# Kernel tuning notes

Measured on AMD Instinct MI355X. Metric: run time of the kernel, lower is better.

## Reference

```python
import jax, jax.numpy as jnp
import numpy as np

B, SQ, SK, D, H, F = 8, 512, 1024, 1024, 16, 4096
DK = D // H
NEG_INF = -jnp.inf


def _linear(x, w, b):
    return x @ w + b


def _mha(q, k, v, wq, bq, wk, bk, wv, bv, wo, bo, causal, kv_mask):
    # q: [B,Sq,D], k/v: [B,Sk,D]
    b, sq, d = q.shape
    sk = k.shape[1]
    Q = _linear(q, wq, bq).reshape(b, sq, H, DK).transpose(0, 2, 1, 3)  # [B,H,Sq,dk]
    K = _linear(k, wk, bk).reshape(b, sk, H, DK).transpose(0, 2, 1, 3)
    V = _linear(v, wv, bv).reshape(b, sk, H, DK).transpose(0, 2, 1, 3)
    S = jnp.einsum('bhqd,bhkd->bhqk', Q, K) / jnp.sqrt(jnp.asarray(DK, Q.dtype))
    if kv_mask is not None:
        S = jnp.where(kv_mask[:, None, None, :] == 0, NEG_INF, S)
    if causal:
        tri = jnp.tril(jnp.ones((sq, sk), dtype=bool))
        S = jnp.where(tri, S, NEG_INF)
    A = jax.nn.softmax(S, axis=-1)  # dropout p=0 -> identity
    x = jnp.einsum('bhqk,bhkd->bhqd', A, V).transpose(0, 2, 1, 3).reshape(b, sq, d)
    return _linear(x, wo, bo), A


def _ln(x, g, beta, eps=1e-5):
    mu = jnp.mean(x, axis=-1, keepdims=True)
    var = jnp.mean(jnp.square(x - mu), axis=-1, keepdims=True)
    return (x - mu) * jax.lax.rsqrt(var + eps) * g + beta


def setup_inputs() -> dict:
    key = jax.random.key(0)
    ks = jax.random.split(key, 32)
    s = 0.02
    inp = {
        'x': jax.random.normal(ks[0], (B, SQ, D), jnp.float32),
        'enc_o': jax.random.normal(ks[1], (B, SK, D), jnp.float32),
        'enc_mask': jax.random.randint(ks[2], (B, SK), 0, 2, jnp.int32),
    }
    i = 3
    for pfx in ('a1', 'a2'):
        for nm in ('wq', 'wk', 'wv', 'wo'):
            inp[f'{pfx}_{nm}'] = jax.random.normal(ks[i], (D, D), jnp.float32) * s; i += 1
            inp[f'{pfx}_{nm[1:] and "b" + nm[1:]}'] = jnp.zeros((D,), jnp.float32)
    inp['ff_w1'] = jax.random.normal(ks[i], (D, F), jnp.float32) * s; i += 1
    inp['ff_b1'] = jnp.zeros((F,), jnp.float32)
    inp['ff_w2'] = jax.random.normal(ks[i], (F, D), jnp.float32) * s; i += 1
    inp['ff_b2'] = jnp.zeros((D,), jnp.float32)
    for n in ('ln1', 'ln2', 'ln3'):
        inp[f'{n}_g'] = jnp.ones((D,), jnp.float32)
        inp[f'{n}_b'] = jnp.zeros((D,), jnp.float32)
    return inp


def reference(x, enc_o, enc_mask,
              a1_wq, a1_bq, a1_wk, a1_bk, a1_wv, a1_bv, a1_wo, a1_bo,
              a2_wq, a2_bq, a2_wk, a2_bk, a2_wv, a2_bv, a2_wo, a2_bo,
              ff_w1, ff_b1, ff_w2, ff_b2,
              ln1_g, ln1_b, ln2_g, ln2_b, ln3_g, ln3_b):
    res, _ = _mha(x, x, x, a1_wq, a1_bq, a1_wk, a1_bk, a1_wv, a1_bv, a1_wo, a1_bo,
                  causal=True, kv_mask=None)
    x = _ln(x + res, ln1_g, ln1_b)
    res, attn = _mha(x, enc_o, enc_o, a2_wq, a2_bq, a2_wk, a2_bk, a2_wv, a2_bv, a2_wo, a2_bo,
                     causal=False, kv_mask=enc_mask)
    x = _ln(x + res, ln2_g, ln2_b)
    res = _linear(jax.nn.relu(_linear(x, ff_w1, ff_b1)), ff_w2, ff_b2)
    x = _ln(x + res, ln3_g, ln3_b)
    return (x, attn)
```

## Files before the change

### kernel.cpp

```cpp
#include <hip/hip_runtime.h>
#include <hip/hip_bf16.h>


using bf16 = __hip_bfloat16;
typedef __attribute__((ext_vector_type(8))) short short8;
typedef __attribute__((ext_vector_type(4))) float f32x4;

#define DEVINL __device__ __forceinline__

DEVINL unsigned short bf16bits(float f) {
  __hip_bfloat16 h = __float2bfloat16(f);
  return *reinterpret_cast<unsigned short*>(&h);
}
DEVINL float bits2f(unsigned short u) {
  return __uint_as_float(((unsigned int)u) << 16);
}
DEVINL float tofloat(float f) { return f; }
DEVINL float tofloat(bf16 h) { return __bfloat162float(h); }

#define GLD16(gp, lp) __builtin_amdgcn_global_load_lds( \
    (__attribute__((address_space(1))) const void*)(gp), \
    (__attribute__((address_space(3))) void*)(lp), 16, 0, 0)

struct GemmP {
  const bf16* A; const bf16* Bt; void* C;
  const float* bias; const int* kmask;
  float scale;
  int M, N, K, lda, ldb, ldc;
  long sAb, sAh, sBb, sBh, sCb, sCh;
};

enum { EPI_BIAS_BF16 = 0, EPI_CAUSAL_BF16, EPI_KMASK_F32, EPI_NONE_BF16,
       EPI_BIAS_F32, EPI_BIAS_RELU_BF16, EPI_PART_F32 };

template<int EPI>
DEVINL void gemm_body(const GemmP& p, int bx, int by, int bz) {
  __shared__ bf16 As[128 * 32];
  __shared__ bf16 Bs[128 * 32];
  const int t = threadIdx.x;
  const int lane = t & 63;
  const int w = t >> 6;
  const int zb = bz >> 4, zh = bz & 15;
  const int m0 = by * 128, n0 = bx * 128;

  const bf16* Ab = p.A + (long)zb * p.sAb + (long)zh * p.sAh;
  const bf16* Bb = p.Bt + (long)zb * p.sBb + (long)zh * p.sBh;
  const int fl = lane & 15, fq = lane >> 4;
  const int wm = (w >> 1) * 64, wn = (w & 1) * 64;

  f32x4 acc[4][4];
#pragma unroll
  for (int i = 0; i < 4; ++i)
#pragma unroll
    for (int j = 0; j < 4; ++j) acc[i][j] = (f32x4){0.f, 0.f, 0.f, 0.f};

  const int sr = t >> 2;
  const int sc = (t & 3) * 8;
  char* ldsA = (char*)As + w * 1024;
  char* ldsB = (char*)Bs + w * 1024;

  int brow0 = n0 + sr;      if (brow0 > p.N - 1) brow0 = p.N - 1;
  int brow1 = n0 + sr + 64; if (brow1 > p.N - 1) brow1 = p.N - 1;

  for (int k0 = 0; k0 < p.K; k0 += 32) {
    GLD16(Ab + (long)(m0 + sr) * p.lda + k0 + sc, ldsA);
    GLD16(Ab + (long)(m0 + sr + 64) * p.lda + k0 + sc, ldsA + 4096);
    GLD16(Bb + (long)brow0 * p.ldb + k0 + sc, ldsB);
    GLD16(Bb + (long)brow1 * p.ldb + k0 + sc, ldsB + 4096);
    __syncthreads();

    short8 af[4], bfv[4];
#pragma unroll
    for (int i = 0; i < 4; ++i)
      af[i] = *(const short8*)(As + (wm + i * 16 + fl) * 32 + fq * 8);
#pragma unroll
    for (int j = 0; j < 4; ++j)
      bfv[j] = *(const short8*)(Bs + (wn + j * 16 + fl) * 32 + fq * 8);
#pragma unroll
    for (int i = 0; i < 4; ++i)
#pragma unroll
      for (int j = 0; j < 4; ++j)
        acc[i][j] = __builtin_amdgcn_mfma_f32_16x16x32_bf16(af[i], bfv[j], acc[i][j], 0, 0, 0);
    __syncthreads();
  }

  const float NEGINF = -__builtin_inff();
  const long cbase = (long)zb * p.sCb + (long)zh * p.sCh;
#pragma unroll
  for (int i = 0; i < 4; ++i) {
#pragma unroll
    for (int j = 0; j < 4; ++j) {
#pragma unroll
      for (int r = 0; r < 4; ++r) {
        int row = m0 + wm + i * 16 + fq * 4 + r;
        int col = n0 + wn + j * 16 + fl;
        if (col < p.N) {
          float v = acc[i][j][r];
          if (EPI == EPI_BIAS_BF16 || EPI == EPI_BIAS_F32 || EPI == EPI_BIAS_RELU_BF16)
            v += p.bias[col];
          if (EPI == EPI_BIAS_RELU_BF16) v = v > 0.f ? v : 0.f;
          if (EPI == EPI_CAUSAL_BF16) { v *= p.scale; if (col > row) v = NEGINF; }
          if (EPI == EPI_KMASK_F32)   { v *= p.scale; if (p.kmask[zb * 1024 + col] == 0) v = NEGINF; }
          long off = cbase + (long)row * p.ldc + col;
          if (EPI == EPI_KMASK_F32 || EPI == EPI_BIAS_F32 || EPI == EPI_PART_F32)
            ((float*)p.C)[off] = v;
          else ((bf16*)p.C)[off] = __float2bfloat16(v);
        }
      }
    }
  }
}

template<int EPI>
__global__ __launch_bounds__(256)
void gemm_k(GemmP p) {
  gemm_body<EPI>(p, blockIdx.x, blockIdx.y, blockIdx.z);
}

struct Gemm2P { GemmP a, b; int nA, axw, bxw; };
__global__ __launch_bounds__(256)
void gemm2_k(Gemm2P q) {
  const int b = blockIdx.x;
  if (b < q.nA) gemm_body<EPI_BIAS_BF16>(q.a, b % q.axw, b / q.axw, 0);
  else { const int c = b - q.nA; gemm_body<EPI_BIAS_BF16>(q.b, c % q.bxw, c / q.bxw, 0); }
}

struct AttnP {
  const bf16 *Q, *K, *Vt;
  float* Pout; bf16* O;
  const int* kmask;
  int ldq, ldk, ldv;
  long sQb, sQh, sKb, sKh, sVb, sVh, sPb, sPh, sOb, sOh;
};

template<int SK, bool CAUSAL, bool WRITE_P>
__global__ __launch_bounds__(512)
void attn_fused_k(AttnP p) {
  constexpr int TKMAX = SK / 64;
  __shared__ bf16 S[64 * SK];
  __shared__ bf16 ring[3 * 4096];
  const int t = threadIdx.x;
  const int lane = t & 63;
  const int w = t >> 6;
  const int fl = lane & 15, fq = lane >> 4;
  const int qh = w >> 2;
  const int wc = w & 3;
  const int zb = blockIdx.z >> 4, zh = blockIdx.z & 15;
  const int q0 = blockIdx.y * 64;
  const float NEGINF = -__builtin_inff();

  const bf16* Qb = p.Q + (long)zb * p.sQb + (long)zh * p.sQh;
  const bf16* Kb = p.K + (long)zb * p.sKb + (long)zh * p.sKh;
  const bf16* Vb = p.Vt + (long)zb * p.sVb + (long)zh * p.sVh;

  const int Tk = CAUSAL ? (q0 >> 6) + 1 : TKMAX;

  short8 af[2][2];
#pragma unroll
  for (int i = 0; i < 2; ++i)
#pragma unroll
    for (int kk = 0; kk < 2; ++kk)
      af[i][kk] = *(const short8*)(Qb + (long)(q0 + qh * 32 + i * 16 + fl) * p.ldq + kk * 32 + fq * 8);

  int kmv[CAUSAL ? 1 : TKMAX];
  if (!CAUSAL) {
#pragma unroll
    for (int kt = 0; kt < TKMAX; ++kt)
      kmv[kt] = p.kmask[zb * 1024 + kt * 64 + wc * 16 + fl];
  }

  const int so = t * 16;
  const int srow = so >> 7;
  const int scb = (so & 127) ^ ((srow & 7) << 4);
  auto stage = [&](const bf16* mb, int ld, int roff, int coff, int buf) {
    GLD16(mb + (long)(roff + srow) * ld + coff + (scb >> 1),
          (char*)ring + buf * 8192 + so);
  };

  stage(Kb, p.ldk, 0, 0, 0);
  if (Tk > 1) stage(Kb, p.ldk, 64, 0, 1);
  for (int kt = 0; kt < Tk; ++kt) {
    if (kt + 1 < Tk) asm volatile("s_waitcnt vmcnt(1)" ::: "memory");
    else             asm volatile("s_waitcnt vmcnt(0)" ::: "memory");
    __builtin_amdgcn_s_barrier();
    if (kt + 2 < Tk) stage(Kb, p.ldk, (kt + 2) * 64, 0, (kt + 2) % 3);

    const char* kb = (const char*)ring + (kt % 3) * 8192;
    const int krow = wc * 16 + fl;
    short8 bfv[2];
#pragma unroll
    for (int kk = 0; kk < 2; ++kk)
      bfv[kk] = *(const short8*)(kb + ((krow * 128 + kk * 64 + fq * 16) ^ ((krow & 7) << 4)));
    f32x4 acc[2] = {(f32x4){0.f,0.f,0.f,0.f}, (f32x4){0.f,0.f,0.f,0.f}};
#pragma unroll
    for (int kk = 0; kk < 2; ++kk) {
      acc[0] = __builtin_amdgcn_mfma_f32_16x16x32_bf16(af[0][kk], bfv[kk], acc[0], 0, 0, 0);
      acc[1] = __builtin_amdgcn_mfma_f32_16x16x32_bf16(af[1][kk], bfv[kk], acc[1], 0, 0, 0);
    }
    const int col = kt * 64 + wc * 16 + fl;
    const bool mok = CAUSAL || (kmv[CAUSAL ? 0 : kt] != 0);
#pragma unroll
    for (int i = 0; i < 2; ++i) {
#pragma unroll
      for (int r = 0; r < 4; ++r) {
        int row = qh * 32 + i * 16 + fq * 4 + r;
        float v = acc[i][r] * 0.125f;
        if (CAUSAL) { if (col > q0 + row) v = NEGINF; }
        else if (!mok) v = NEGINF;
        int b = ((row * SK + col) * 2) ^ ((row & 7) << 4);
        *(bf16*)((char*)S + b) = __float2bfloat16(v);
      }
    }
  }
  asm volatile("s_waitcnt lgkmcnt(0)" ::: "memory");
  __builtin_amdgcn_s_barrier();

  const int Tv = Tk;
  stage(Vb, p.ldv, 0, 0, 0);
  if (Tv > 1) stage(Vb, p.ldv, 0, 64, 1);

  float* Pf = WRITE_P ? (p.Pout + (long)zb * p.sPb + (long)zh * p.sPh) : nullptr;
  constexpr int NC = SK / 512;
  const int lim = Tk * 64;
  for (int rr = 0; rr < 8; ++rr) {
    const int row = w * 8 + rr;
    const int swz = (row & 7) << 4;
    float fv[NC][8];
#pragma unroll
    for (int c = 0; c < NC; ++c) {
      const int col = c * 512 + lane * 8;
      if (!CAUSAL || col < lim) {
        short8 sv = *(const short8*)((char*)S + (((row * SK + col) * 2) ^ swz));
#pragma unroll
        for (int j = 0; j < 8; ++j) fv[c][j] = bits2f((unsigned short)sv[j]);
      } else {
#pragma unroll
        for (int j = 0; j < 8; ++j) fv[c][j] = NEGINF;
      }
    }
    float mx = fv[0][0];
#pragma unroll
    for (int c = 0; c < NC; ++c)
#pragma unroll
      for (int j = 0; j < 8; ++j) mx = fmaxf(mx, fv[c][j]);
    for (int off = 32; off; off >>= 1) mx = fmaxf(mx, __shfl_xor(mx, off, 64));
    float s = 0.f;
#pragma unroll
    for (int c = 0; c < NC; ++c)
#pragma unroll
      for (int j = 0; j < 8; ++j) { fv[c][j] = expf(fv[c][j] - mx); s += fv[c][j]; }
    for (int off = 32; off; off >>= 1) s += __shfl_xor(s, off, 64);
    const float inv = 1.f / s;
#pragma unroll
    for (int c = 0; c < NC; ++c) {
      const int col = c * 512 + lane * 8;
      if (!CAUSAL || col < lim) {
        short8 o;
#pragma unroll
        for (int j = 0; j < 8; ++j) o[j] = (short)bf16bits(fv[c][j] * inv);
        *(short8*)((char*)S + (((row * SK + col) * 2) ^ swz)) = o;
        if (WRITE_P) {
          float* pp = Pf + (long)(q0 + row) * SK + col;
          f32x4 o0, o1;
#pragma unroll
          for (int j = 0; j < 4; ++j) { o0[j] = fv[c][j] * inv; o1[j] = fv[c][4 + j] * inv; }
          *(f32x4*)pp = o0;
          *(f32x4*)(pp + 4) = o1;
        }
      }
    }
  }
  asm volatile("s_waitcnt lgkmcnt(0)" ::: "memory");
  __builtin_amdgcn_s_barrier();

  f32x4 ao[2] = {(f32x4){0.f,0.f,0.f,0.f}, (f32x4){0.f,0.f,0.f,0.f}};
  for (int vt = 0; vt < Tv; ++vt) {
    if (vt + 1 < Tv) asm volatile("s_waitcnt vmcnt(1)" ::: "memory");
    else             asm volatile("s_waitcnt vmcnt(0)" ::: "memory");
    __builtin_amdgcn_s_barrier();
    if (vt + 2 < Tv) stage(Vb, p.ldv, 0, (vt + 2) * 64, (vt + 2) % 3);

    const char* vbuf = (const char*)ring + (vt % 3) * 8192;
    const int vrow = wc * 16 + fl;
    short8 bv[2];
#pragma unroll
    for (int kk = 0; kk < 2; ++kk)
      bv[kk] = *(const short8*)(vbuf + ((vrow * 128 + kk * 64 + fq * 16) ^ ((vrow & 7) << 4)));
#pragma unroll
    for (int i = 0; i < 2; ++i) {
      const int row = qh * 32 + i * 16 + fl;
#pragma unroll
      for (int kk = 0; kk < 2; ++kk) {
        const int col = vt * 64 + kk * 32 + fq * 8;
        short8 pa = *(const short8*)((char*)S + (((row * SK + col) * 2) ^ ((row & 7) << 4)));
        ao[i] = __builtin_amdgcn_mfma_f32_16x16x32_bf16(pa, bv[kk], ao[i], 0, 0, 0);
      }
    }
  }

  bf16* Ob_ = p.O + (long)zb * p.sOb + (long)zh * p.sOh;
#pragma unroll
  for (int i = 0; i < 2; ++i)
#pragma unroll
    for (int r = 0; r < 4; ++r) {
      int row = q0 + qh * 32 + i * 16 + fq * 4 + r;
      Ob_[(long)row * 1024 + wc * 16 + fl] = __float2bfloat16(ao[i][r]);
    }
}

template<int NP>
__global__ __launch_bounds__(256)
void ln_fuse_k(const float* __restrict__ x, const float* __restrict__ part, long pstride,
               const float* __restrict__ pb,
               const float* __restrict__ g, const float* __restrict__ bt,
               float* __restrict__ outf, bf16* __restrict__ outb) {
  const int lane = threadIdx.x & 63;
  const long row = (long)blockIdx.x * 4 + (threadIdx.x >> 6);
  const float* px = x + row * 1024;
  float4 v[4];
  float s = 0.f;
#pragma unroll
  for (int c = 0; c < 4; ++c) {
    const int col = c * 256 + lane * 4;
    float4 a = *(const float4*)(px + col);
    float4 bb = *(const float4*)(pb + col);
    v[c].x = a.x + bb.x; v[c].y = a.y + bb.y; v[c].z = a.z + bb.z; v[c].w = a.w + bb.w;
#pragma unroll
    for (int sl = 0; sl < NP; ++sl) {
      float4 pp = *(const float4*)(part + sl * pstride + row * 1024 + col);
      v[c].x += pp.x; v[c].y += pp.y; v[c].z += pp.z; v[c].w += pp.w;
    }
    s += v[c].x + v[c].y + v[c].z + v[c].w;
  }
  for (int off = 32; off; off >>= 1) s += __shfl_xor(s, off, 64);
  float mu = s * (1.f / 1024.f);
  float q = 0.f;
#pragma unroll
  for (int c = 0; c < 4; ++c) {
    float dx = v[c].x - mu, dy = v[c].y - mu, dz = v[c].z - mu, dw = v[c].w - mu;
    q += dx * dx + dy * dy + dz * dz + dw * dw;
  }
  for (int off = 32; off; off >>= 1) q += __shfl_xor(q, off, 64);
  float rs = rsqrtf(q * (1.f / 1024.f) + 1e-5f);
#pragma unroll
  for (int c = 0; c < 4; ++c) {
    int col = c * 256 + lane * 4;
    float4 gg = *(const float4*)(g + col);
    float4 bb = *(const float4*)(bt + col);
    float4 o;
    o.x = (v[c].x - mu) * rs * gg.x + bb.x;
    o.y = (v[c].y - mu) * rs * gg.y + bb.y;
    o.z = (v[c].z - mu) * rs * gg.z + bb.z;
    o.w = (v[c].w - mu) * rs * gg.w + bb.w;
    *(float4*)(outf + row * 1024 + col) = o;
    if (outb) {
      uint2 pk;
      pk.x = bf16bits(o.x) | ((unsigned)bf16bits(o.y) << 16);
      pk.y = bf16bits(o.z) | ((unsigned)bf16bits(o.w) << 16);
      *(uint2*)(outb + row * 1024 + col) = pk;
    }
  }
}

template<typename TI>
DEVINL void tr_body(const TI* __restrict__ pin, bf16* __restrict__ pout,
                    int ldi, int ldo, int c0, int r0, int t, float tile[32][33]) {
  const int tx = t & 31, ty = t >> 5;
#pragma unroll
  for (int i = 0; i < 32; i += 8)
    tile[ty + i][tx] = tofloat(pin[(long)(r0 + ty + i) * ldi + c0 + tx]);
  __syncthreads();
#pragma unroll
  for (int i = 0; i < 32; i += 8)
    pout[(long)(c0 + ty + i) * ldo + r0 + tx] = __float2bfloat16(tile[tx][ty + i]);
}

struct PrepP {
  const float *x, *enc;
  const float* wsrc[10];
  const float *b0, *b1, *b2, *b4, *b5;
  bf16 *xb, *encb, *wT;
  float *bqkv, *bkv;
};
__global__ __launch_bounds__(256)
void prep_k(PrepP p) {
  __shared__ float tile[32][33];
  const int b = blockIdx.x, t = threadIdx.x;
  if (b < 12288) {
    const float* src = (b < 4096) ? p.x : p.enc;
    bf16* dst = (b < 4096) ? p.xb : p.encb;
    long i = (long)(b < 4096 ? b : b - 4096) * 256 + t;
    float4 v = *(const float4*)(src + i * 4);
    uint2 pk;
    pk.x = bf16bits(v.x) | ((unsigned)bf16bits(v.y) << 16);
    pk.y = bf16bits(v.z) | ((unsigned)bf16bits(v.w) << 16);
    *(uint2*)(dst + i * 4) = pk;
  } else if (b < 20480) {
    int l = b - 12288; int wdx = l >> 10; l &= 1023;
    tr_body<float>(p.wsrc[wdx], p.wT + (long)wdx * 1048576, 1024, 1024,
                   (l & 31) * 32, (l >> 5) * 32, t, tile);
  } else if (b < 24576) {
    int l = b - 20480;
    tr_body<float>(p.wsrc[8], p.wT + 8l * 1048576, 4096, 1024,
                   (l & 127) * 32, (l >> 7) * 32, t, tile);
  } else if (b < 28672) {
    int l = b - 24576;
    tr_body<float>(p.wsrc[9], p.wT + 12l * 1048576, 1024, 4096,
                   (l % 32) * 32, (l / 32) * 32, t, tile);
  } else if (b < 28684) {
    int i = (b - 28672) * 256 + t;
    p.bqkv[i] = (i < 1024) ? p.b0[i] : (i < 2048 ? p.b1[i - 1024] : p.b2[i - 2048]);
  } else {
    int i = (b - 28684) * 256 + t;
    p.bkv[i] = (i < 1024) ? p.b4[i] : p.b5[i - 1024];
  }
}

struct Vt2P { const bf16 *vs, *vc; bf16 *vts, *vtc; };
__global__ __launch_bounds__(256)
void vt2_k(Vt2P p) {
  __shared__ float tile[32][33];
  const int b = blockIdx.x, t = threadIdx.x;
  if (b < 4096) {
    int z = b >> 5, l = b & 31;
    int zb = z >> 4, zh = z & 15;
    tr_body<bf16>(p.vs + (long)zb * 1572864 + zh * 64,
                  p.vts + (long)zb * 524288 + zh * 32768,
                  3072, 512, (l & 1) * 32, (l >> 1) * 32, t, tile);
  } else {
    int c = b - 4096;
    int z = c >> 6, l = c & 63;
    int zb = z >> 4, zh = z & 15;
    tr_body<bf16>(p.vc + (long)zb * 2097152 + zh * 64,
                  p.vtc + (long)zb * 1048576 + zh * 65536,
                  2048, 1024, (l & 1) * 32, (l >> 1) * 32, t, tile);
  }
}

static inline GemmP mkp(const void* A, const bf16* Bt, void* C,
                        const float* bias, const int* km, float sc,
                        int M, int N, int K, int lda, int ldb, int ldc,
                        long sAb, long sAh, long sBb, long sBh, long sCb, long sCh) {
  GemmP p;
  p.A = (const bf16*)A; p.Bt = Bt; p.C = C; p.bias = bias; p.kmask = km; p.scale = sc;
  p.M = M; p.N = N; p.K = K; p.lda = lda; p.ldb = ldb; p.ldc = ldc;
  p.sAb = sAb; p.sAh = sAh; p.sBb = sBb; p.sBh = sBh; p.sCb = sCb; p.sCh = sCh;
  return p;
}

extern "C" void kernel_launch(void* const* d_in, const int* in_sizes, int n_in,
                              void* d_out, int out_size, void* d_ws, size_t ws_size,
                              hipStream_t stream) {
  const float* x        = (const float*)d_in[0];
  const float* enc_o    = (const float*)d_in[1];
  const int*   enc_mask = (const int*)d_in[2];
  const float* a1_wq = (const float*)d_in[3];  const float* a1_bq = (const float*)d_in[4];
  const float* a1_wk = (const float*)d_in[5];  const float* a1_bk = (const float*)d_in[6];
  const float* a1_wv = (const float*)d_in[7];  const float* a1_bv = (const float*)d_in[8];
  const float* a1_wo = (const float*)d_in[9];  const float* a1_bo = (const float*)d_in[10];
  const float* a2_wq = (const float*)d_in[11]; const float* a2_bq = (const float*)d_in[12];
  const float* a2_wk = (const float*)d_in[13]; const float* a2_bk = (const float*)d_in[14];
  const float* a2_wv = (const float*)d_in[15]; const float* a2_bv = (const float*)d_in[16];
  const float* a2_wo = (const float*)d_in[17]; const float* a2_bo = (const float*)d_in[18];
  const float* ff_w1 = (const float*)d_in[19]; const float* ff_b1 = (const float*)d_in[20];
  const float* ff_w2 = (const float*)d_in[21]; const float* ff_b2 = (const float*)d_in[22];
  const float* ln1_g = (const float*)d_in[23]; const float* ln1_b = (const float*)d_in[24];
  const float* ln2_g = (const float*)d_in[25]; const float* ln2_b = (const float*)d_in[26];
  const float* ln3_g = (const float*)d_in[27]; const float* ln3_b = (const float*)d_in[28];

  const size_t MB = 1u << 20;
  const long M1 = 1048576;
  char* w = (char*)d_ws;
  bf16*  xb   = (bf16*)(w + 0);
  bf16*  encb = (bf16*)(w + 8 * MB);
  float* x1f  = (float*)(w + 24 * MB);
  float* x2f  = (float*)(w + 40 * MB);
  bf16*  xcb  = (bf16*)(w + 56 * MB);
  bf16*  wT   = (bf16*)(w + 64 * MB);
  float* bqkv = (float*)(w + 96 * MB);
  float* bkv  = (float*)(w + 96 * MB + 16384);
  bf16*  QKV  = (bf16*)(w + 104 * MB);
  bf16*  KVc  = (bf16*)(w + 128 * MB);
  bf16*  VtS  = (bf16*)(w + 160 * MB);
  bf16*  Ob   = (bf16*)(w + 176 * MB);
  float* part = (float*)(w + 200 * MB);
  bf16*  Asf  = (bf16*)(w + 264 * MB);
  bf16*  VtC  = (bf16*)(w + 332 * MB);

  float* out_x = (float*)d_out;
  float* attn  = (float*)d_out + 4194304;

  const dim3 blk(256);
  const dim3 blk5(512);

  {
    PrepP pp;
    pp.x = x; pp.enc = enc_o;
    pp.wsrc[0] = a1_wq; pp.wsrc[1] = a1_wk; pp.wsrc[2] = a1_wv; pp.wsrc[3] = a1_wo;
    pp.wsrc[4] = a2_wq; pp.wsrc[5] = a2_wk; pp.wsrc[6] = a2_wv; pp.wsrc[7] = a2_wo;
    pp.wsrc[8] = ff_w1; pp.wsrc[9] = ff_w2;
    pp.b0 = a1_bq; pp.b1 = a1_bk; pp.b2 = a1_bv; pp.b4 = a2_bk; pp.b5 = a2_bv;
    pp.xb = xb; pp.encb = encb; pp.wT = wT; pp.bqkv = bqkv; pp.bkv = bkv;
    prep_k<<<28692, blk, 0, stream>>>(pp);
  }

  {
    Gemm2P q;
    q.a = mkp(xb, wT, QKV, bqkv, nullptr, 0.f, 4096, 3072, 1024, 1024, 1024, 3072, 0,0,0,0,0,0);
    q.b = mkp(encb, wT + 5 * M1, KVc, bkv, nullptr, 0.f, 8192, 2048, 1024, 1024, 1024, 2048, 0,0,0,0,0,0);
    q.nA = 768; q.axw = 24; q.bxw = 16;
    gemm2_k<<<1792, blk, 0, stream>>>(q);
  }
  bf16* Qs = QKV;
  bf16* Ks = QKV + 1024;
  bf16* Vs = QKV + 2048;
  bf16* Kc = KVc;
  bf16* Vc = KVc + 1024;

  {
    Vt2P vp; vp.vs = Vs; vp.vc = Vc; vp.vts = VtS; vp.vtc = VtC;
    vt2_k<<<12288, blk, 0, stream>>>(vp);
  }

  {
    AttnP ap;
    ap.Q = Qs; ap.K = Ks; ap.Vt = VtS; ap.Pout = nullptr; ap.O = Ob; ap.kmask = nullptr;
    ap.ldq = 3072; ap.ldk = 3072; ap.ldv = 512;
    ap.sQb = 1572864; ap.sQh = 64; ap.sKb = 1572864; ap.sKh = 64;
    ap.sVb = 524288;  ap.sVh = 32768; ap.sPb = 0; ap.sPh = 0;
    ap.sOb = 524288;  ap.sOh = 64;
    attn_fused_k<512, true, false><<<dim3(1, 8, 128), blk5, 0, stream>>>(ap);
  }

  gemm_k<EPI_PART_F32><<<dim3(8, 32, 2), blk, 0, stream>>>(
      mkp(Ob, wT + 3 * M1, part, nullptr, nullptr, 0.f, 4096, 1024, 512, 1024, 1024, 1024,
          0, 512, 0, 512, 0, 4194304));

  ln_fuse_k<2><<<1024, blk, 0, stream>>>(x, part, 4194304, a1_bo, ln1_g, ln1_b, x1f, xcb);

  gemm_k<EPI_BIAS_BF16><<<dim3(8, 32, 1), blk, 0, stream>>>(
      mkp(xcb, wT + 4 * M1, QKV, a2_bq, nullptr, 0.f, 4096, 1024, 1024, 1024, 1024, 1024, 0,0,0,0,0,0));
  bf16* Qc = QKV;

  {
    AttnP ap;
    ap.Q = Qc; ap.K = Kc; ap.Vt = VtC; ap.Pout = attn; ap.O = Ob; ap.kmask = enc_mask;
    ap.ldq = 1024; ap.ldk = 2048; ap.ldv = 1024;
    ap.sQb = 524288;  ap.sQh = 64; ap.sKb = 2097152; ap.sKh = 64;
    ap.sVb = 1048576; ap.sVh = 65536; ap.sPb = 8388608; ap.sPh = 524288;
    ap.sOb = 524288;  ap.sOh = 64;
    attn_fused_k<1024, false, true><<<dim3(1, 8, 128), blk5, 0, stream>>>(ap);
  }

  gemm_k<EPI_PART_F32><<<dim3(8, 32, 2), blk, 0, stream>>>(
      mkp(Ob, wT + 7 * M1, part, nullptr, nullptr, 0.f, 4096, 1024, 512, 1024, 1024, 1024,
          0, 512, 0, 512, 0, 4194304));

  ln_fuse_k<2><<<1024, blk, 0, stream>>>(x1f, part, 4194304, a2_bo, ln2_g, ln2_b, x2f, xcb);

  gemm_k<EPI_BIAS_RELU_BF16><<<dim3(32, 32, 1), blk, 0, stream>>>(
      mkp(xcb, wT + 8 * M1, Asf, ff_b1, nullptr, 0.f, 4096, 4096, 1024, 1024, 1024, 4096, 0,0,0,0,0,0));

  gemm_k<EPI_PART_F32><<<dim3(8, 32, 4), blk, 0, stream>>>(
      mkp(Asf, wT + 12 * M1, part, nullptr, nullptr, 0.f, 4096, 1024, 1024, 4096, 4096, 1024,
          0, 1024, 0, 1024, 0, 4194304));

  ln_fuse_k<4><<<1024, blk, 0, stream>>>(x2f, part, 4194304, ff_b2, ln3_g, ln3_b, out_x, nullptr);
}
```

Baseline: 988.8 us.

## Halve attention query tile, remap grid across XCDs, use nontemporal stores for P

Each attention block now handles 32 query rows instead of 64. This halves the shared score buffer and cuts the K/V ring from triple to double buffering, so more blocks can be resident per CU. The launch becomes a 1D grid of 2048 blocks, remapped so that neighbouring heads and tiles are spread across XCDs. The fp32 attention-probability output now uses nontemporal stores. The cost is that each K/V tile is loaded twice as often across blocks, and each tile step gains an extra barrier.

```diff
diff --git a/kernel.cpp b/kernel.cpp
--- a/kernel.cpp
+++ b/kernel.cpp
@@ -137,16 +137,20 @@
 __global__ __launch_bounds__(512)
 void attn_fused_k(AttnP p) {
   constexpr int TKMAX = SK / 64;
-  __shared__ bf16 S[64 * SK];
-  __shared__ bf16 ring[3 * 4096];
+  __shared__ bf16 S[32 * SK];
+  __shared__ bf16 ring[2 * 4096];
   const int t = threadIdx.x;
   const int lane = t & 63;
   const int w = t >> 6;
   const int fl = lane & 15, fq = lane >> 4;
   const int qh = w >> 2;
   const int wc = w & 3;
-  const int zb = blockIdx.z >> 4, zh = blockIdx.z & 15;
-  const int q0 = blockIdx.y * 64;
+  const int lin = blockIdx.x;
+  const int wg = (lin & 7) * 256 + (lin >> 3);
+  const int by = wg & 15;
+  const int z = wg >> 4;
+  const int zb = z >> 4, zh = z & 15;
+  const int q0 = by * 32;
   const float NEGINF = -__builtin_inff();
 
   const bf16* Qb = p.Q + (long)zb * p.sQb + (long)zh * p.sQh;
@@ -155,12 +159,10 @@
 
   const int Tk = CAUSAL ? (q0 >> 6) + 1 : TKMAX;
 
-  short8 af[2][2];
-#pragma unroll
-  for (int i = 0; i < 2; ++i)
-#pragma unroll
-    for (int kk = 0; kk < 2; ++kk)
-      af[i][kk] = *(const short8*)(Qb + (long)(q0 + qh * 32 + i * 16 + fl) * p.ldq + kk * 32 + fq * 8);
+  short8 af[2];
+#pragma unroll
+  for (int kk = 0; kk < 2; ++kk)
+    af[kk] = *(const short8*)(Qb + (long)(q0 + qh * 16 + fl) * p.ldq + kk * 32 + fq * 8);
 
   int kmv[CAUSAL ? 1 : TKMAX];
   if (!CAUSAL) {
@@ -183,37 +185,31 @@
     if (kt + 1 < Tk) asm volatile("s_waitcnt vmcnt(1)" ::: "memory");
     else             asm volatile("s_waitcnt vmcnt(0)" ::: "memory");
     __builtin_amdgcn_s_barrier();
-    if (kt + 2 < Tk) stage(Kb, p.ldk, (kt + 2) * 64, 0, (kt + 2) % 3);
-
-    const char* kb = (const char*)ring + (kt % 3) * 8192;
+
+    const char* kb = (const char*)ring + (kt & 1) * 8192;
     const int krow = wc * 16 + fl;
     short8 bfv[2];
 #pragma unroll
     for (int kk = 0; kk < 2; ++kk)
       bfv[kk] = *(const short8*)(kb + ((krow * 128 + kk * 64 + fq * 16) ^ ((krow & 7) << 4)));
-    f32x4 acc[2] = {(f32x4){0.f,0.f,0.f,0.f}, (f32x4){0.f,0.f,0.f,0.f}};
-#pragma unroll
-    for (int kk = 0; kk < 2; ++kk) {
-      acc[0] = __builtin_amdgcn_mfma_f32_16x16x32_bf16(af[0][kk], bfv[kk], acc[0], 0, 0, 0);
-      acc[1] = __builtin_amdgcn_mfma_f32_16x16x32_bf16(af[1][kk], bfv[kk], acc[1], 0, 0, 0);
-    }
-    const int col = kt * 64 + wc * 16 + fl;
+    f32x4 acc = (f32x4){0.f, 0.f, 0.f, 0.f};
+#pragma unroll
+    for (int kk = 0; kk < 2; ++kk)
+      acc = __builtin_amdgcn_mfma_f32_16x16x32_bf16(af[kk], bfv[kk], acc, 0, 0, 0);
+    const int col = kt * 64 + krow;
     const bool mok = CAUSAL || (kmv[CAUSAL ? 0 : kt] != 0);
 #pragma unroll
-    for (int i = 0; i < 2; ++i) {
-#pragma unroll
-      for (int r = 0; r < 4; ++r) {
-        int row = qh * 32 + i * 16 + fq * 4 + r;
-        float v = acc[i][r] * 0.125f;
-        if (CAUSAL) { if (col > q0 + row) v = NEGINF; }
-        else if (!mok) v = NEGINF;
-        int b = ((row * SK + col) * 2) ^ ((row & 7) << 4);
-        *(bf16*)((char*)S + b) = __float2bfloat16(v);
-      }
-    }
-  }
-  asm volatile("s_waitcnt lgkmcnt(0)" ::: "memory");
-  __builtin_amdgcn_s_barrier();
+    for (int r = 0; r < 4; ++r) {
+      int row = qh * 16 + fq * 4 + r;
+      float v = acc[r] * 0.125f;
+      if (CAUSAL) { if (col > q0 + row) v = NEGINF; }
+      else if (!mok) v = NEGINF;
+      *(bf16*)((char*)S + (((row * SK + col) * 2) ^ ((row & 7) << 4))) = __float2bfloat16(v);
+    }
+    asm volatile("s_waitcnt lgkmcnt(0)" ::: "memory");
+    __builtin_amdgcn_s_barrier();
+    if (kt + 2 < Tk) stage(Kb, p.ldk, (kt + 2) * 64, 0, kt & 1);
+  }
 
   const int Tv = Tk;
   stage(Vb, p.ldv, 0, 0, 0);
@@ -222,8 +218,9 @@
   float* Pf = WRITE_P ? (p.Pout + (long)zb * p.sPb + (long)zh * p.sPh) : nullptr;
   constexpr int NC = SK / 512;
   const int lim = Tk * 64;
-  for (int rr = 0; rr < 8; ++rr) {
-    const int row = w * 8 + rr;
+  for (int rr = 0; rr < 4; ++rr) {
+    const int row = w * 4 + rr;
+    const int rg = q0 + row;
     const int swz = (row & 7) << 4;
     float fv[NC][8];
 #pragma unroll
@@ -260,12 +257,12 @@
         for (int j = 0; j < 8; ++j) o[j] = (short)bf16bits(fv[c][j] * inv);
         *(short8*)((char*)S + (((row * SK + col) * 2) ^ swz)) = o;
         if (WRITE_P) {
-          float* pp = Pf + (long)(q0 + row) * SK + col;
+          float* pp = Pf + (long)rg * SK + col;
           f32x4 o0, o1;
 #pragma unroll
           for (int j = 0; j < 4; ++j) { o0[j] = fv[c][j] * inv; o1[j] = fv[c][4 + j] * inv; }
-          *(f32x4*)pp = o0;
-          *(f32x4*)(pp + 4) = o1;
+          __builtin_nontemporal_store(o0, (f32x4*)pp);
+          __builtin_nontemporal_store(o1, (f32x4*)(pp + 4));
         }
       }
     }
@@ -273,39 +270,36 @@
   asm volatile("s_waitcnt lgkmcnt(0)" ::: "memory");
   __builtin_amdgcn_s_barrier();
 
-  f32x4 ao[2] = {(f32x4){0.f,0.f,0.f,0.f}, (f32x4){0.f,0.f,0.f,0.f}};
+  f32x4 ao = (f32x4){0.f, 0.f, 0.f, 0.f};
   for (int vt = 0; vt < Tv; ++vt) {
     if (vt + 1 < Tv) asm volatile("s_waitcnt vmcnt(1)" ::: "memory");
     else             asm volatile("s_waitcnt vmcnt(0)" ::: "memory");
     __builtin_amdgcn_s_barrier();
-    if (vt + 2 < Tv) stage(Vb, p.ldv, 0, (vt + 2) * 64, (vt + 2) % 3);
-
-    const char* vbuf = (const char*)ring + (vt % 3) * 8192;
+
+    const char* vbuf = (const char*)ring + (vt & 1) * 8192;
     const int vrow = wc * 16 + fl;
     short8 bv[2];
 #pragma unroll
     for (int kk = 0; kk < 2; ++kk)
       bv[kk] = *(const short8*)(vbuf + ((vrow * 128 + kk * 64 + fq * 16) ^ ((vrow & 7) << 4)));
-#pragma unroll
-    for (int i = 0; i < 2; ++i) {
-      const int row = qh * 32 + i * 16 + fl;
-#pragma unroll
-      for (int kk = 0; kk < 2; ++kk) {
-        const int col = vt * 64 + kk * 32 + fq * 8;
-        short8 pa = *(const short8*)((char*)S + (((row * SK + col) * 2) ^ ((row & 7) << 4)));
-        ao[i] = __builtin_amdgcn_mfma_f32_16x16x32_bf16(pa, bv[kk], ao[i], 0, 0, 0);
-      }
-    }
+    const int prow = qh * 16 + fl;
+#pragma unroll
+    for (int kk = 0; kk < 2; ++kk) {
+      const int col = vt * 64 + kk * 32 + fq * 8;
+      short8 pa = *(const short8*)((char*)S + (((prow * SK + col) * 2) ^ ((prow & 7) << 4)));
+      ao = __builtin_amdgcn_mfma_f32_16x16x32_bf16(pa, bv[kk], ao, 0, 0, 0);
+    }
+    asm volatile("s_waitcnt lgkmcnt(0)" ::: "memory");
+    __builtin_amdgcn_s_barrier();
+    if (vt + 2 < Tv) stage(Vb, p.ldv, 0, (vt + 2) * 64, vt & 1);
   }
 
   bf16* Ob_ = p.O + (long)zb * p.sOb + (long)zh * p.sOh;
 #pragma unroll
-  for (int i = 0; i < 2; ++i)
-#pragma unroll
-    for (int r = 0; r < 4; ++r) {
-      int row = q0 + qh * 32 + i * 16 + fq * 4 + r;
-      Ob_[(long)row * 1024 + wc * 16 + fl] = __float2bfloat16(ao[i][r]);
-    }
+  for (int r = 0; r < 4; ++r) {
+    int row = q0 + qh * 16 + fq * 4 + r;
+    Ob_[(long)row * 1024 + wc * 16 + fl] = __float2bfloat16(ao[r]);
+  }
 }
 
 template<int NP>
@@ -529,7 +523,7 @@
     ap.sQb = 1572864; ap.sQh = 64; ap.sKb = 1572864; ap.sKh = 64;
     ap.sVb = 524288;  ap.sVh = 32768; ap.sPb = 0; ap.sPh = 0;
     ap.sOb = 524288;  ap.sOh = 64;
-    attn_fused_k<512, true, false><<<dim3(1, 8, 128), blk5, 0, stream>>>(ap);
+    attn_fused_k<512, true, false><<<dim3(2048), blk5, 0, stream>>>(ap);
   }
 
   gemm_k<EPI_PART_F32><<<dim3(8, 32, 2), blk, 0, stream>>>(
@@ -549,7 +543,7 @@
     ap.sQb = 524288;  ap.sQh = 64; ap.sKb = 2097152; ap.sKh = 64;
     ap.sVb = 1048576; ap.sVh = 65536; ap.sPb = 8388608; ap.sPh = 524288;
     ap.sOb = 524288;  ap.sOh = 64;
-    attn_fused_k<1024, false, true><<<dim3(1, 8, 128), blk5, 0, stream>>>(ap);
+    attn_fused_k<1024, false, true><<<dim3(2048), blk5, 0, stream>>>(ap);
   }
 
   gemm_k<EPI_PART_F32><<<dim3(8, 32, 2), blk, 0, stream>>>(
```

New measurement: 982.3 us. About the same (-0.7%).
